# Kernel optimization log

Measured on AMD Instinct MI355X. Metric: run time of the kernel, lower is better.

The kernel has to match this reference:

```python
import jax, jax.numpy as jnp
import numpy as np

N_OBS = 8_000_000
N_CAM = 2_000
N_PTS = 1_000_000


def _rotate_quat(points, qt):
    """Rotate points by unit quaternion qt[...,:4]=(w,x,y,z), then translate by qt[...,4:7]."""
    q = qt[..., :4]
    q = q / jnp.linalg.norm(q, axis=-1, keepdims=True)
    w = q[..., :1]          # [N,1]
    v = q[..., 1:4]         # [N,3]
    # p' = p + 2*v x (v x p + w*p)
    t = jnp.cross(v, points) + w * points
    rotated = points + 2.0 * jnp.cross(v, t)
    return rotated + qt[..., 4:7]


def _project(points, camera_params):
    p = _rotate_quat(points, camera_params[..., :7])          # [N,3]
    proj = -p[..., :2] / p[..., 2:3]                          # perspective divide, [N,2]
    f = camera_params[..., 7:8]
    k1 = camera_params[..., 8:9]
    k2 = camera_params[..., 9:10]
    n = jnp.sum(proj * proj, axis=-1, keepdims=True)          # [N,1]
    r = 1.0 + k1 * n + k2 * n * n                             # radial distortion
    return proj * r * f


def setup_inputs() -> dict:
    key = jax.random.key(0)
    k1, k2, k3, k4, k5 = jax.random.split(key, 5)
    camera_params = jax.random.normal(k1, (N_CAM, 10), dtype=jnp.float32)
    # push translation z away from zero so the perspective divide is well-conditioned
    camera_params = camera_params.at[:, 6].add(5.0)
    points_3d = jax.random.normal(k2, (N_PTS, 3), dtype=jnp.float32)
    points_2d = jax.random.normal(k3, (N_OBS, 2), dtype=jnp.float32)
    camera_indices = jax.random.randint(k4, (N_OBS,), 0, N_CAM, dtype=jnp.int32)
    point_indices = jax.random.randint(k5, (N_OBS,), 0, N_PTS, dtype=jnp.int32)
    return {
        "points_2d": points_2d,
        "camera_indices": camera_indices,
        "point_indices": point_indices,
        "camera_params": camera_params,
        "points_3d": points_3d,
    }


def reference(points_2d, camera_indices, point_indices, camera_params, points_3d):
    pts = points_3d[point_indices]           # gather [N,3]
    cams = camera_params[camera_indices]     # gather [N,10]
    points_proj = _project(pts, cams)        # [N,2]
    return points_proj - points_2d
```

## Files before the change

### kernel.cpp

```cpp
#include <hip/hip_runtime.h>


typedef __attribute__((ext_vector_type(4))) float f32x4;
typedef __attribute__((ext_vector_type(2))) int   i32x2;

#define MAX_CAM_WORDS 20000

__global__ void repack_pts_kernel(const float* __restrict__ pts,
                                  f32x4* __restrict__ out, int npts) {
    int i = blockIdx.x * blockDim.x + threadIdx.x;
    if (i < npts) {
        const float* p = pts + (size_t)i * 3;
        f32x4 v = {p[0], p[1], p[2], 0.0f};
        out[i] = v;
    }
}

__device__ __forceinline__ float2 project_one(
    const float* lds_cams, int ci,
    float pxf, float pyf, float pzf,
    float obsx, float obsy)
{
    const float2* cl = reinterpret_cast<const float2*>(lds_cams + ci * 10);
    float2 c01 = cl[0];
    float2 c23 = cl[1];
    float2 c45 = cl[2];
    float2 c67 = cl[3];
    float2 c89 = cl[4];

    double px = (double)pxf, py = (double)pyf, pz = (double)pzf;
    double qw = (double)c01.x, qx = (double)c01.y;
    double qy = (double)c23.x, qz = (double)c23.y;

    double nrm2 = qw * qw + qx * qx + qy * qy + qz * qz;
    double s = 1.0 / sqrt(nrm2);
    double w  = qw * s;
    double vx = qx * s, vy = qy * s, vz = qz * s;

    double tx = (vy * pz - vz * py) + w * px;
    double ty = (vz * px - vx * pz) + w * py;
    double tz = (vx * py - vy * px) + w * pz;

    double X = (px + 2.0 * (vy * tz - vz * ty)) + (double)c45.x;
    double Y = (py + 2.0 * (vz * tx - vx * tz)) + (double)c45.y;
    double Z = (pz + 2.0 * (vx * ty - vy * tx)) + (double)c67.x;

    double rz  = 1.0 / Z;
    double prx = -X * rz;
    double pry = -Y * rz;

    double f  = (double)c67.y;
    double k1 = (double)c89.x, k2 = (double)c89.y;

    double nn = prx * prx + pry * pry;
    double r  = 1.0 + k1 * nn + k2 * nn * nn;
    double rf = r * f;

    float2 o;
    o.x = (float)(prx * rf - (double)obsx);
    o.y = (float)(pry * rf - (double)obsy);
    return o;
}

__global__ __launch_bounds__(1024, 8) void reproj_kernel(
    const f32x4*  __restrict__ p2d4,
    const int*    __restrict__ cam_idx,
    const int*    __restrict__ pt_idx,
    const float*  __restrict__ cams,
    const float*  __restrict__ pts_raw,
    const f32x4*  __restrict__ pts_packed,
    f32x4*        __restrict__ out4,
    int n, int ncam_words)
{
    __shared__ float lds_cams[MAX_CAM_WORDS];

    {
        int nv = ncam_words >> 2;
        if (nv > (MAX_CAM_WORDS >> 2)) nv = MAX_CAM_WORDS >> 2;
        const f32x4* src = reinterpret_cast<const f32x4*>(cams);
        f32x4* dst = reinterpret_cast<f32x4*>(lds_cams);
        for (int j = threadIdx.x; j < nv; j += blockDim.x)
            dst[j] = src[j];
        for (int j = (nv << 2) + threadIdx.x; j < ncam_words && j < MAX_CAM_WORDS;
             j += blockDim.x)
            lds_cams[j] = cams[j];
    }
    __syncthreads();

    int i = (blockIdx.x * blockDim.x + threadIdx.x) * 2;
    if (i + 1 < n) {
        i32x2 ci = __builtin_nontemporal_load(
            reinterpret_cast<const i32x2*>(cam_idx + i));
        i32x2 pi = __builtin_nontemporal_load(
            reinterpret_cast<const i32x2*>(pt_idx + i));
        f32x4 ob = __builtin_nontemporal_load(p2d4 + (i >> 1));

        float ax, ay, az, bx, by, bz;
        if (pts_packed) {
            f32x4 pa = pts_packed[pi.x];
            f32x4 pb = pts_packed[pi.y];
            ax = pa.x; ay = pa.y; az = pa.z;
            bx = pb.x; by = pb.y; bz = pb.z;
        } else {
            const float* pA = pts_raw + (size_t)pi.x * 3;
            const float* pB = pts_raw + (size_t)pi.y * 3;
            ax = pA[0]; ay = pA[1]; az = pA[2];
            bx = pB[0]; by = pB[1]; bz = pB[2];
        }

        float2 o0 = project_one(lds_cams, ci.x, ax, ay, az, ob.x, ob.y);
        float2 o1 = project_one(lds_cams, ci.y, bx, by, bz, ob.z, ob.w);
        f32x4 ov = {o0.x, o0.y, o1.x, o1.y};
        __builtin_nontemporal_store(ov, out4 + (i >> 1));
    } else if (i < n) {
        int ci = cam_idx[i];
        int pi = pt_idx[i];
        float ax, ay, az;
        if (pts_packed) {
            f32x4 pa = pts_packed[pi];
            ax = pa.x; ay = pa.y; az = pa.z;
        } else {
            const float* pA = pts_raw + (size_t)pi * 3;
            ax = pA[0]; ay = pA[1]; az = pA[2];
        }
        const float* p2 = reinterpret_cast<const float*>(p2d4);
        float2 o = project_one(lds_cams, ci, ax, ay, az,
                               p2[2 * i], p2[2 * i + 1]);
        float* po = reinterpret_cast<float*>(out4);
        po[2 * i]     = o.x;
        po[2 * i + 1] = o.y;
    }
}

extern "C" void kernel_launch(void* const* d_in, const int* in_sizes, int n_in,
                              void* d_out, int out_size, void* d_ws, size_t ws_size,
                              hipStream_t stream) {
    const float* p2d     = (const float*)d_in[0];
    const int*   cam_idx = (const int*)d_in[1];
    const int*   pt_idx  = (const int*)d_in[2];
    const float* cams    = (const float*)d_in[3];
    const float* pts     = (const float*)d_in[4];

    int n    = in_sizes[1];
    int ncw  = in_sizes[3];
    int npts = in_sizes[4] / 3;

    f32x4* packed = nullptr;
    if (ws_size >= (size_t)npts * 16) {
        packed = (f32x4*)d_ws;
        int t = 256;
        int b = (npts + t - 1) / t;
        repack_pts_kernel<<<b, t, 0, stream>>>(pts, packed, npts);
    }

    int threads = 1024;
    int per_block = threads * 2;
    int blocks = (n + per_block - 1) / per_block;

    reproj_kernel<<<blocks, threads, 0, stream>>>(
        (const f32x4*)p2d, cam_idx, pt_idx, cams, pts, packed,
        (f32x4*)d_out, n, ncw);
}
```

Measured before the change: 155.8 us.

## Drop LDS camera staging, read cameras from global cache, four obs per thread

Removes the per-block copy of the whole 80KB camera table into shared memory and the barrier that follows it, and reads camera parameters straight from global memory, relying on L1/L2 caching. Each thread now handles four observations using 128-bit index loads, with 256-thread blocks instead of 1024. The repack kernel writes with nontemporal stores. This trades redundant per-block LDS fills and low occupancy for uncached scattered global camera reads.

```diff
diff --git a/kernel.cpp b/kernel.cpp
--- a/kernel.cpp
+++ b/kernel.cpp
@@ -2,9 +2,7 @@
 
 
 typedef __attribute__((ext_vector_type(4))) float f32x4;
-typedef __attribute__((ext_vector_type(2))) int   i32x2;
-
-#define MAX_CAM_WORDS 20000
+typedef __attribute__((ext_vector_type(4))) int   i32x4;
 
 __global__ void repack_pts_kernel(const float* __restrict__ pts,
                                   f32x4* __restrict__ out, int npts) {
@@ -12,16 +10,16 @@
     if (i < npts) {
         const float* p = pts + (size_t)i * 3;
         f32x4 v = {p[0], p[1], p[2], 0.0f};
-        out[i] = v;
+        __builtin_nontemporal_store(v, out + i);
     }
 }
 
 __device__ __forceinline__ float2 project_one(
-    const float* lds_cams, int ci,
+    const float* __restrict__ cams, int ci,
     float pxf, float pyf, float pzf,
     float obsx, float obsy)
 {
-    const float2* cl = reinterpret_cast<const float2*>(lds_cams + ci * 10);
+    const float2* cl = reinterpret_cast<const float2*>(cams + (size_t)ci * 10);
     float2 c01 = cl[0];
     float2 c23 = cl[1];
     float2 c45 = cl[2];
@@ -62,7 +60,7 @@
     return o;
 }
 
-__global__ __launch_bounds__(1024, 8) void reproj_kernel(
+__global__ __launch_bounds__(256) void reproj_kernel(
     const f32x4*  __restrict__ p2d4,
     const int*    __restrict__ cam_idx,
     const int*    __restrict__ pt_idx,
@@ -70,65 +68,64 @@
     const float*  __restrict__ pts_raw,
     const f32x4*  __restrict__ pts_packed,
     f32x4*        __restrict__ out4,
-    int n, int ncam_words)
+    int n)
 {
-    __shared__ float lds_cams[MAX_CAM_WORDS];
+    int base = (blockIdx.x * blockDim.x + threadIdx.x) * 4;
 
-    {
-        int nv = ncam_words >> 2;
-        if (nv > (MAX_CAM_WORDS >> 2)) nv = MAX_CAM_WORDS >> 2;
-        const f32x4* src = reinterpret_cast<const f32x4*>(cams);
-        f32x4* dst = reinterpret_cast<f32x4*>(lds_cams);
-        for (int j = threadIdx.x; j < nv; j += blockDim.x)
-            dst[j] = src[j];
-        for (int j = (nv << 2) + threadIdx.x; j < ncam_words && j < MAX_CAM_WORDS;
-             j += blockDim.x)
-            lds_cams[j] = cams[j];
-    }
-    __syncthreads();
+    if (base + 3 < n) {
+        i32x4 ci = __builtin_nontemporal_load(
+            reinterpret_cast<const i32x4*>(cam_idx + base));
+        i32x4 pi = __builtin_nontemporal_load(
+            reinterpret_cast<const i32x4*>(pt_idx + base));
 
-    int i = (blockIdx.x * blockDim.x + threadIdx.x) * 2;
-    if (i + 1 < n) {
-        i32x2 ci = __builtin_nontemporal_load(
-            reinterpret_cast<const i32x2*>(cam_idx + i));
-        i32x2 pi = __builtin_nontemporal_load(
-            reinterpret_cast<const i32x2*>(pt_idx + i));
-        f32x4 ob = __builtin_nontemporal_load(p2d4 + (i >> 1));
-
-        float ax, ay, az, bx, by, bz;
+        f32x4 p0, p1, p2, p3;
         if (pts_packed) {
-            f32x4 pa = pts_packed[pi.x];
-            f32x4 pb = pts_packed[pi.y];
-            ax = pa.x; ay = pa.y; az = pa.z;
-            bx = pb.x; by = pb.y; bz = pb.z;
+            p0 = pts_packed[pi.x];
+            p1 = pts_packed[pi.y];
+            p2 = pts_packed[pi.z];
+            p3 = pts_packed[pi.w];
         } else {
-            const float* pA = pts_raw + (size_t)pi.x * 3;
-            const float* pB = pts_raw + (size_t)pi.y * 3;
-            ax = pA[0]; ay = pA[1]; az = pA[2];
-            bx = pB[0]; by = pB[1]; bz = pB[2];
+            const float* a = pts_raw + (size_t)pi.x * 3;
+            const float* b = pts_raw + (size_t)pi.y * 3;
+            const float* c = pts_raw + (size_t)pi.z * 3;
+            const float* d = pts_raw + (size_t)pi.w * 3;
+            p0 = {a[0], a[1], a[2], 0.f};
+            p1 = {b[0], b[1], b[2], 0.f};
+            p2 = {c[0], c[1], c[2], 0.f};
+            p3 = {d[0], d[1], d[2], 0.f};
         }
 
-        float2 o0 = project_one(lds_cams, ci.x, ax, ay, az, ob.x, ob.y);
-        float2 o1 = project_one(lds_cams, ci.y, bx, by, bz, ob.z, ob.w);
-        f32x4 ov = {o0.x, o0.y, o1.x, o1.y};
-        __builtin_nontemporal_store(ov, out4 + (i >> 1));
-    } else if (i < n) {
-        int ci = cam_idx[i];
-        int pi = pt_idx[i];
-        float ax, ay, az;
-        if (pts_packed) {
-            f32x4 pa = pts_packed[pi];
-            ax = pa.x; ay = pa.y; az = pa.z;
-        } else {
-            const float* pA = pts_raw + (size_t)pi * 3;
-            ax = pA[0]; ay = pA[1]; az = pA[2];
+        f32x4 obA = __builtin_nontemporal_load(p2d4 + (base >> 1));
+        f32x4 obB = __builtin_nontemporal_load(p2d4 + (base >> 1) + 1);
+
+        float2 o0 = project_one(cams, ci.x, p0.x, p0.y, p0.z, obA.x, obA.y);
+        float2 o1 = project_one(cams, ci.y, p1.x, p1.y, p1.z, obA.z, obA.w);
+        f32x4 ovA = {o0.x, o0.y, o1.x, o1.y};
+        __builtin_nontemporal_store(ovA, out4 + (base >> 1));
+
+        float2 o2 = project_one(cams, ci.z, p2.x, p2.y, p2.z, obB.x, obB.y);
+        float2 o3 = project_one(cams, ci.w, p3.x, p3.y, p3.z, obB.z, obB.w);
+        f32x4 ovB = {o2.x, o2.y, o3.x, o3.y};
+        __builtin_nontemporal_store(ovB, out4 + (base >> 1) + 1);
+    } else {
+        const float* p2 = reinterpret_cast<const float*>(p2d4);
+        float* po = reinterpret_cast<float*>(out4);
+        for (int i = base; i < n; ++i) {
+            int ci = cam_idx[i];
+            int pi = pt_idx[i];
+            float ax, ay, az;
+            if (pts_packed) {
+                f32x4 pa = pts_packed[pi];
+                ax = pa.x; ay = pa.y; az = pa.z;
+            } else {
+                const float* pA = pts_raw + (size_t)pi * 3;
+                ax = pA[0]; ay = pA[1]; az = pA[2];
+            }
+            float2 o = project_one(cams, ci, ax, ay, az,
+                                   p2[2 * i], p2[2 * i + 1]);
+            po[2 * i]     = o.x;
+            po[2 * i + 1] = o.y;
         }
-        const float* p2 = reinterpret_cast<const float*>(p2d4);
-        float2 o = project_one(lds_cams, ci, ax, ay, az,
-                               p2[2 * i], p2[2 * i + 1]);
-        float* po = reinterpret_cast<float*>(out4);
-        po[2 * i]     = o.x;
-        po[2 * i + 1] = o.y;
     }
 }
 
@@ -142,7 +139,6 @@
     const float* pts     = (const float*)d_in[4];
 
     int n    = in_sizes[1];
-    int ncw  = in_sizes[3];
     int npts = in_sizes[4] / 3;
 
     f32x4* packed = nullptr;
@@ -153,11 +149,11 @@
         repack_pts_kernel<<<b, t, 0, stream>>>(pts, packed, npts);
     }
 
-    int threads = 1024;
-    int per_block = threads * 2;
+    int threads = 256;
+    int per_block = threads * 4;
     int blocks = (n + per_block - 1) / per_block;
 
     reproj_kernel<<<blocks, threads, 0, stream>>>(
         (const f32x4*)p2d, cam_idx, pt_idx, cams, pts, packed,
-        (f32x4*)d_out, n, ncw);
+        (f32x4*)d_out, n);
 }
```

New measurement: 194.0 us. 1.25x slower.
